# Kernel tuning notes

Measured on AMD Instinct MI355X. Metric: run time of the kernel, lower is better.

The kernel has to match this reference:

```python
import jax, jax.numpy as jnp
import numpy as np

B, S = 8192, 32
N_NODES, N_EDGES = 200000, 500000
D_NODE = D_EDGE = 172
D_TIME = 100
D_IN = D_NODE + D_NODE + D_EDGE + D_TIME  # 616


def setup_inputs() -> dict:
    key = jax.random.key(0)
    ks = jax.random.split(key, 16)
    node_raw_features = jax.random.normal(ks[0], (N_NODES, D_NODE), dtype=jnp.float32)
    edge_raw_features = jax.random.normal(ks[1], (N_EDGES, D_EDGE), dtype=jnp.float32)
    src_node_ids = jax.random.randint(ks[2], (B,), 0, N_NODES)
    dst_node_ids = jax.random.randint(ks[3], (B,), 0, N_NODES)
    node_interact_times = jax.random.uniform(ks[4], (B,), dtype=jnp.float32) * 1000.0
    src_nbr_ids = jax.random.randint(ks[5], (B, S), 0, N_NODES)
    src_edge_ids = jax.random.randint(ks[6], (B, S), 0, N_EDGES)
    src_nbr_times = jax.random.uniform(ks[7], (B, S), dtype=jnp.float32) * 1000.0
    dst_nbr_ids = jax.random.randint(ks[8], (B, S), 0, N_NODES)
    dst_edge_ids = jax.random.randint(ks[9], (B, S), 0, N_EDGES)
    dst_nbr_times = jax.random.uniform(ks[10], (B, S), dtype=jnp.float32) * 1000.0
    # TimeEncoder: frozen Linear(1, D_TIME) with w = 1/10^linspace(0,9,D_TIME), b = 0
    time_w = (1.0 / (10.0 ** jnp.linspace(0.0, 9.0, D_TIME))).astype(jnp.float32)
    time_b = jnp.zeros((D_TIME,), dtype=jnp.float32)
    W_out = jax.random.normal(ks[11], (D_IN, D_NODE), dtype=jnp.float32) * 0.02
    b_out = jnp.zeros((D_NODE,), dtype=jnp.float32)
    return {
        "node_raw_features": node_raw_features,
        "edge_raw_features": edge_raw_features,
        "src_node_ids": src_node_ids,
        "dst_node_ids": dst_node_ids,
        "node_interact_times": node_interact_times,
        "src_nbr_ids": src_nbr_ids,
        "src_edge_ids": src_edge_ids,
        "src_nbr_times": src_nbr_times,
        "dst_nbr_ids": dst_nbr_ids,
        "dst_edge_ids": dst_edge_ids,
        "dst_nbr_times": dst_nbr_times,
        "time_w": time_w,
        "time_b": time_b,
        "W_out": W_out,
        "b_out": b_out,
    }


def _side_embedding(node_raw_features, edge_raw_features, node_ids, interact_times,
                    nbr_ids, edge_ids, nbr_times, time_w, time_b, W_out, b_out):
    nf = node_raw_features[nbr_ids]            # [B,S,D_NODE] gather
    ef = edge_raw_features[edge_ids]           # [B,S,D_EDGE] gather
    dt = interact_times[:, None] - nbr_times   # [B,S]
    tf = jnp.cos(dt[..., None] * time_w + time_b)  # [B,S,D_TIME]
    tf = jnp.where((nbr_ids == 0)[..., None], 0.0, tf)  # zero padded-time features
    combined = jnp.concatenate([nf, ef, tf], axis=-1)   # [B,S,D_NODE+D_EDGE+D_TIME]
    agg = combined.mean(axis=1)                          # mean over padded seq (divide by S)
    cur = node_raw_features[node_ids]                    # [B,D_NODE]
    inp = jnp.concatenate([cur, agg], axis=-1)           # [B,D_IN]
    return jax.nn.relu(inp @ W_out + b_out)              # dropout is identity in eval


def reference(node_raw_features, edge_raw_features, src_node_ids, dst_node_ids,
              node_interact_times, src_nbr_ids, src_edge_ids, src_nbr_times,
              dst_nbr_ids, dst_edge_ids, dst_nbr_times, time_w, time_b, W_out, b_out):
    src_emb = _side_embedding(node_raw_features, edge_raw_features, src_node_ids,
                              node_interact_times, src_nbr_ids, src_edge_ids,
                              src_nbr_times, time_w, time_b, W_out, b_out)
    dst_emb = _side_embedding(node_raw_features, edge_raw_features, dst_node_ids,
                              node_interact_times, dst_nbr_ids, dst_edge_ids,
                              dst_nbr_times, time_w, time_b, W_out, b_out)
    dummy = jnp.zeros_like(src_emb)
    return src_emb, dst_emb, dummy
```

## Files before the change

### kernel.cpp

```cpp
#include <hip/hip_runtime.h>

#define ROWS  16
#define BLOCK 256
#define PAD   620

__global__ __launch_bounds__(BLOCK) void spe_fused(
    const float* __restrict__ nodef,
    const float* __restrict__ edgef,
    const int*   __restrict__ src_ids,
    const int*   __restrict__ dst_ids,
    const float* __restrict__ itimes,
    const int*   __restrict__ s_nbr,
    const int*   __restrict__ s_eid,
    const float* __restrict__ s_t,
    const int*   __restrict__ d_nbr,
    const int*   __restrict__ d_eid,
    const float* __restrict__ d_t,
    const float* __restrict__ tw,
    const float* __restrict__ tb,
    const float* __restrict__ W,
    const float* __restrict__ bout,
    float*       __restrict__ out)
{
    __shared__ float inp[ROWS * PAD];
    __shared__ int   noff[ROWS * 32];
    __shared__ int   eoff[ROWS * 32];
    __shared__ float dtm[ROWS * 32];
    __shared__ float msk[ROWS * 32];
    __shared__ int   curoff[ROWS];
    __shared__ float twl[100], tbl[100];

    const int tid     = threadIdx.x;
    const int side    = blockIdx.x >> 9;
    const int rowbase = (blockIdx.x & 511) * ROWS;

    const int*   nbr  = side ? d_nbr : s_nbr;
    const int*   eidp = side ? d_eid : s_eid;
    const float* ntp  = side ? d_t   : s_t;
    const int*   nids = side ? dst_ids : src_ids;

    for (int i = tid; i < ROWS * 32; i += BLOCK) {
        int g   = rowbase * 32 + i;
        int nid = nbr[g];
        noff[i] = nid * 172;
        eoff[i] = eidp[g] * 172;
        dtm[i]  = itimes[rowbase + (i >> 5)] - ntp[g];
        msk[i]  = (nid == 0) ? 0.f : 1.f;
    }
    if (tid < ROWS) curoff[tid] = nids[rowbase + tid] * 172;
    if (tid < 100) { twl[tid] = tw[tid]; tbl[tid] = tb[tid]; }
    __syncthreads();

    for (int i = tid; i < ROWS * 172; i += BLOCK) {
        int r = i / 172, d = i - r * 172;
        inp[r * PAD + d] = nodef[curoff[r] + d];
    }

    for (int i = tid; i < ROWS * 444; i += BLOCK) {
        int r = i / 444, d = i - r * 444;
        const int rb = r * 32;
        float acc = 0.f;
        if (d < 344) {
            const float* bp;
            const int*   offp;
            int dd;
            if (d < 172) { bp = nodef; offp = noff; dd = d; }
            else         { bp = edgef; offp = eoff; dd = d - 172; }
            #pragma unroll
            for (int s = 0; s < 32; ++s) acc += bp[offp[rb + s] + dd];
            inp[r * PAD + 172 + d] = acc * (1.f / 32.f);
        } else {
            int j = d - 344;
            float w = twl[j], b = tbl[j];
            #pragma unroll
            for (int s = 0; s < 32; ++s)
                acc += msk[rb + s] * __cosf(dtm[rb + s] * w + b);
            inp[r * PAD + 516 + j] = acc * (1.f / 32.f);
        }
    }
    __syncthreads();

    if (tid < 172) {
        const int ct = tid % 43, rt = tid / 43;
        const int j0 = ct * 4, r0 = rt * 4;
        float acc[4][4] = {};
        float a[4][4];
        for (int k = 0; k < 616; k += 4) {
            #pragma unroll
            for (int ri = 0; ri < 4; ++ri)
                *(float4*)&a[ri][0] = *(const float4*)&inp[(r0 + ri) * PAD + k];
            #pragma unroll
            for (int kk = 0; kk < 4; ++kk) {
                float4 wv = *(const float4*)&W[(k + kk) * 172 + j0];
                #pragma unroll
                for (int ri = 0; ri < 4; ++ri) {
                    acc[ri][0] += a[ri][kk] * wv.x;
                    acc[ri][1] += a[ri][kk] * wv.y;
                    acc[ri][2] += a[ri][kk] * wv.z;
                    acc[ri][3] += a[ri][kk] * wv.w;
                }
            }
        }
        float4 bias = *(const float4*)&bout[j0];
        #pragma unroll
        for (int ri = 0; ri < 4; ++ri) {
            int row = rowbase + r0 + ri;
            float4 v;
            v.x = fmaxf(acc[ri][0] + bias.x, 0.f);
            v.y = fmaxf(acc[ri][1] + bias.y, 0.f);
            v.z = fmaxf(acc[ri][2] + bias.z, 0.f);
            v.w = fmaxf(acc[ri][3] + bias.w, 0.f);
            *(float4*)&out[(size_t)(side * 8192 + row) * 172 + j0] = v;
        }
    }

    if (side == 0) {
        for (int i = tid; i < ROWS * 172; i += BLOCK) {
            int r = i / 172, d = i - r * 172;
            out[(size_t)(2 * 8192 + rowbase + r) * 172 + d] = 0.f;
        }
    }
}

extern "C" void kernel_launch(void* const* d_in, const int* in_sizes, int n_in,
                              void* d_out, int out_size, void* d_ws, size_t ws_size,
                              hipStream_t stream) {
    const float* nodef   = (const float*)d_in[0];
    const float* edgef   = (const float*)d_in[1];
    const int*   src_ids = (const int*)  d_in[2];
    const int*   dst_ids = (const int*)  d_in[3];
    const float* itimes  = (const float*)d_in[4];
    const int*   s_nbr   = (const int*)  d_in[5];
    const int*   s_eid   = (const int*)  d_in[6];
    const float* s_t     = (const float*)d_in[7];
    const int*   d_nbr   = (const int*)  d_in[8];
    const int*   d_eid   = (const int*)  d_in[9];
    const float* d_t     = (const float*)d_in[10];
    const float* tw      = (const float*)d_in[11];
    const float* tb      = (const float*)d_in[12];
    const float* W       = (const float*)d_in[13];
    const float* bout    = (const float*)d_in[14];
    float* out = (float*)d_out;

    spe_fused<<<1024, BLOCK, 0, stream>>>(
        nodef, edgef, src_ids, dst_ids, itimes,
        s_nbr, s_eid, s_t, d_nbr, d_eid, d_t,
        tw, tb, W, bout, out);
}
```

Baseline: 255.5 us.

## Vectorize neighbor gathers to float4 with batched loads and split aggregation loops

Rewrites the node, edge and current-row gathers and the zero fill to use float4 loads and stores, one thread per 4 columns. Each gather thread issues 8 independent row loads before summing, to raise memory-level parallelism. The time-encoding loop is separated from the gather loops to remove the per-element branch. Launch bounds now request 3 blocks per SM, which may limit registers and risks spills given the 8-wide float4 buffers and the 16-accumulator GEMM.

```diff
diff --git a/kernel.cpp b/kernel.cpp
--- a/kernel.cpp
+++ b/kernel.cpp
@@ -4,7 +4,7 @@
 #define BLOCK 256
 #define PAD   620
 
-__global__ __launch_bounds__(BLOCK) void spe_fused(
+__global__ __launch_bounds__(BLOCK, 3) void spe_fused(
     const float* __restrict__ nodef,
     const float* __restrict__ edgef,
     const int*   __restrict__ src_ids,
@@ -51,32 +51,63 @@
     if (tid < 100) { twl[tid] = tw[tid]; tbl[tid] = tb[tid]; }
     __syncthreads();
 
-    for (int i = tid; i < ROWS * 172; i += BLOCK) {
-        int r = i / 172, d = i - r * 172;
-        inp[r * PAD + d] = nodef[curoff[r] + d];
+    for (int i = tid; i < ROWS * 43; i += BLOCK) {
+        int r = i / 43, c = i - r * 43;
+        *(float4*)&inp[r * PAD + 4 * c] =
+            *(const float4*)&nodef[curoff[r] + 4 * c];
     }
 
-    for (int i = tid; i < ROWS * 444; i += BLOCK) {
-        int r = i / 444, d = i - r * 444;
+    for (int i = tid; i < ROWS * 43; i += BLOCK) {
+        int r = i / 43, c = i - r * 43;
+        const int dd = 4 * c, rb = r * 32;
+        float4 acc = {0.f, 0.f, 0.f, 0.f};
+        #pragma unroll
+        for (int s0 = 0; s0 < 32; s0 += 8) {
+            float4 v[8];
+            #pragma unroll
+            for (int u = 0; u < 8; ++u)
+                v[u] = *(const float4*)&nodef[noff[rb + s0 + u] + dd];
+            #pragma unroll
+            for (int u = 0; u < 8; ++u) {
+                acc.x += v[u].x; acc.y += v[u].y;
+                acc.z += v[u].z; acc.w += v[u].w;
+            }
+        }
+        acc.x *= (1.f/32.f); acc.y *= (1.f/32.f);
+        acc.z *= (1.f/32.f); acc.w *= (1.f/32.f);
+        *(float4*)&inp[r * PAD + 172 + dd] = acc;
+    }
+
+    for (int i = tid; i < ROWS * 43; i += BLOCK) {
+        int r = i / 43, c = i - r * 43;
+        const int dd = 4 * c, rb = r * 32;
+        float4 acc = {0.f, 0.f, 0.f, 0.f};
+        #pragma unroll
+        for (int s0 = 0; s0 < 32; s0 += 8) {
+            float4 v[8];
+            #pragma unroll
+            for (int u = 0; u < 8; ++u)
+                v[u] = *(const float4*)&edgef[eoff[rb + s0 + u] + dd];
+            #pragma unroll
+            for (int u = 0; u < 8; ++u) {
+                acc.x += v[u].x; acc.y += v[u].y;
+                acc.z += v[u].z; acc.w += v[u].w;
+            }
+        }
+        acc.x *= (1.f/32.f); acc.y *= (1.f/32.f);
+        acc.z *= (1.f/32.f); acc.w *= (1.f/32.f);
+        *(float4*)&inp[r * PAD + 344 + dd] = acc;
+    }
+
+    for (int i = tid; i < ROWS * 100; i += BLOCK) {
+        int r = i / 100, j = i - r * 100;
         const int rb = r * 32;
+        float w = twl[j], b = tbl[j];
         float acc = 0.f;
-        if (d < 344) {
-            const float* bp;
-            const int*   offp;
-            int dd;
-            if (d < 172) { bp = nodef; offp = noff; dd = d; }
-            else         { bp = edgef; offp = eoff; dd = d - 172; }
-            #pragma unroll
-            for (int s = 0; s < 32; ++s) acc += bp[offp[rb + s] + dd];
-            inp[r * PAD + 172 + d] = acc * (1.f / 32.f);
-        } else {
-            int j = d - 344;
-            float w = twl[j], b = tbl[j];
-            #pragma unroll
-            for (int s = 0; s < 32; ++s)
-                acc += msk[rb + s] * __cosf(dtm[rb + s] * w + b);
-            inp[r * PAD + 516 + j] = acc * (1.f / 32.f);
-        }
+        #pragma unroll
+        for (int s = 0; s < 32; ++s)
+            acc += msk[rb + s] * __cosf(dtm[rb + s] * w + b);
+        inp[r * PAD + 516 + j] = acc * (1.f / 32.f);
     }
     __syncthreads();
 
@@ -115,9 +146,10 @@
     }
 
     if (side == 0) {
-        for (int i = tid; i < ROWS * 172; i += BLOCK) {
-            int r = i / 172, d = i - r * 172;
-            out[(size_t)(2 * 8192 + rowbase + r) * 172 + d] = 0.f;
+        const float4 z = {0.f, 0.f, 0.f, 0.f};
+        for (int i = tid; i < ROWS * 43; i += BLOCK) {
+            int r = i / 43, c = i - r * 43;
+            *(float4*)&out[(size_t)(2 * 8192 + rowbase + r) * 172 + 4 * c] = z;
         }
     }
 }
```

Measured after the change: 238.8 us. -6.5%, faster.
